# Kernel optimization log

Hardware: AMD Instinct MI355X
Metric: run time of the kernel (lower is better)

Reference implementation:

```python
import jax, jax.numpy as jnp
import numpy as np

B, S, V, I, H = 32, 512, 8000, 256, 512
LN_EPS = 1e-5


def setup_inputs() -> dict:
    key = jax.random.key(0)
    ks = jax.random.split(key, 8)
    norm = lambda k, shp, sc: jax.random.normal(k, shp, dtype=jnp.float32) * sc
    return {
        "x_idx": jax.random.randint(ks[0], (B, S), 0, V),
        "emb": norm(ks[1], (V, I), 1.0),                    # nn.Embedding weight
        "W_in": norm(ks[2], (H, I), 1.0 / np.sqrt(I)),       # input_proj
        "b_in": jnp.zeros((H,), jnp.float32),
        "W_rec": norm(ks[3], (H, H), 1.0 / np.sqrt(H)),      # recurrent_proj
        "b_rec": jnp.zeros((H,), jnp.float32),
        "W_tr": norm(ks[4], (H, H), 1.0 / np.sqrt(H)),       # trunk linear
        "b_tr": jnp.zeros((H,), jnp.float32),
        "gamma": jnp.ones((H,), jnp.float32),                # shared LayerNorm
        "beta": jnp.zeros((H,), jnp.float32),
        "W_out": norm(ks[5], (V, H), 1.0 / np.sqrt(H)),      # output_proj
        "b_out": jnp.zeros((V,), jnp.float32),
    }


def reference(x_idx, emb, W_in, b_in, W_rec, b_rec, W_tr, b_tr, gamma, beta, W_out, b_out):
    bsz = x_idx.shape[0]

    def layer_norm(x):
        m = jnp.mean(x, axis=-1, keepdims=True)
        v = jnp.mean((x - m) ** 2, axis=-1, keepdims=True)
        return (x - m) * jax.lax.rsqrt(v + LN_EPS) * gamma + beta

    xs = emb[x_idx]                     # [B,S,I] gather all embeddings up front
    xs_t = jnp.swapaxes(xs, 0, 1)       # [S,B,I] for scan over time

    def step(h, x_t):
        h_t = jnp.tanh(x_t @ W_in.T + b_in + h @ W_rec.T + b_rec)   # [B,H]
        h_new = layer_norm(jnp.tanh(h_t @ W_tr.T + b_tr))           # trunk (layer_count=1)
        return h_new, h_new

    h0 = jnp.zeros((bsz, W_in.shape[0]), xs.dtype)
    _, hs = jax.lax.scan(step, h0, xs_t)                            # hs: [S,B,H]

    # output projection is out of the recurrence -> batch it after the scan
    y_s = jnp.einsum('sbh,vh->bsv', hs, W_out) + b_out              # [B,S,V]
    return y_s
```

## Files before the change

kernel.cpp:

```cpp
#include <hip/hip_runtime.h>
#include <hip/hip_bf16.h>

#define B_ 32
#define S_ 512
#define V_ 8000
#define I_ 256
#define H_ 512
#define LN_EPS 1e-5f
#define NSL 16
#define NBP 8
#define NBLK 128
#define PHALF (NBLK * 2048)

#define OFF_WR   0
#define OFF_WT   16512
#define OFF_HB   33024
#define OFF_HTS  35088
#define OFF_RED  35220
#define OFF_RED2 37268
#define OFF_MISC 37284
#define LDSF     37288

typedef __attribute__((ext_vector_type(4))) float f32x4;
typedef __attribute__((ext_vector_type(8))) short short8;

static __device__ __forceinline__ unsigned short f2bf(float x) {
    __hip_bfloat16 h = __float2bfloat16(x);
    return *reinterpret_cast<unsigned short*>(&h);
}

__global__ void k_transpose(const float* __restrict__ in, float* __restrict__ out,
                            int R, int C) {
    __shared__ float tile[32][33];
    int c0 = blockIdx.x * 32, r0 = blockIdx.y * 32;
    int tx = threadIdx.x, ty = threadIdx.y;
#pragma unroll
    for (int i = 0; i < 32; i += 8)
        tile[ty + i][tx] = in[(size_t)(r0 + ty + i) * C + (c0 + tx)];
    __syncthreads();
#pragma unroll
    for (int i = 0; i < 32; i += 8)
        out[(size_t)(c0 + ty + i) * R + (r0 + tx)] = tile[tx][ty + i];
}

__global__ __launch_bounds__(256) void k_cvt_bf16(const float* __restrict__ in,
                                                  unsigned short* __restrict__ out, int n4) {
    for (int i = blockIdx.x * 256 + threadIdx.x; i < n4; i += gridDim.x * 256) {
        float4 v = ((const float4*)in)[i];
        ushort4 o;
        o.x = f2bf(v.x); o.y = f2bf(v.y); o.z = f2bf(v.z); o.w = f2bf(v.w);
        ((ushort4*)out)[i] = o;
    }
}

__global__ __launch_bounds__(512) void k_embed_proj(
        const int* __restrict__ x_idx, const float* __restrict__ emb,
        const float* __restrict__ WinT, const float* __restrict__ b_in,
        float* __restrict__ Xp) {
    __shared__ float e[8][I_];
    const int m0 = blockIdx.x * 8;
    const int t = threadIdx.x;
    {
        int r = t >> 6, i4 = (t & 63) * 4;
        int m = m0 + r;
        int s = m >> 5, b = m & 31;
        int idx = x_idx[b * S_ + s];
        *(float4*)&e[r][i4] = *(const float4*)&emb[(size_t)idx * I_ + i4];
    }
    __syncthreads();
    const int j = t;
    float acc[8];
    const float bj = b_in[j];
#pragma unroll
    for (int r = 0; r < 8; ++r) acc[r] = bj;
    for (int i = 0; i < I_; ++i) {
        float w = WinT[(size_t)i * H_ + j];
#pragma unroll
        for (int r = 0; r < 8; ++r) acc[r] += e[r][i] * w;
    }
#pragma unroll
    for (int r = 0; r < 8; ++r)
        Xp[(size_t)(m0 + r) * H_ + j] = acc[r];
}

__global__ __launch_bounds__(512, 2) void k_scan_xcd2(
        const float* __restrict__ Xp,
        const float* __restrict__ W_rec, const float* __restrict__ b_rec,
        const float* __restrict__ W_tr,  const float* __restrict__ b_tr,
        const float* __restrict__ gamma, const float* __restrict__ beta,
        float* __restrict__ pP, unsigned int* __restrict__ flags,
        unsigned int* __restrict__ xccs, unsigned short* __restrict__ hsB) {
    extern __shared__ float sm[];
    float*  WrS  = sm + OFF_WR;
    float*  WtS  = sm + OFF_WT;
    float*  hb   = sm + OFF_HB;
    float*  hts  = sm + OFF_HTS;
    float*  red  = sm + OFF_RED;
    float2* red2 = (float2*)(sm + OFF_RED2);

    const int bid = blockIdx.x;
    const int g = bid >> 3, bp = bid & 7;
    const int t = threadIdx.x;
    const int j = t & 31, kc = t >> 5;
    const int rB = t >> 7, jB = (t & 127) << 2;
    const int wid = t >> 6;

    for (int idx = t; idx < 32 * 512; idx += 512) {
        int jj = idx >> 9, k = idx & 511;
        WrS[jj * 516 + k] = W_rec[(size_t)(g * 32 + jj) * H_ + k];
    }
    for (int idx = t; idx < 512 * 32; idx += 512) {
        int jj = idx >> 5, kl = idx & 31;
        WtS[kl * 516 + jj] = W_tr[(size_t)jj * H_ + g * 32 + kl];
    }
    const float brj = b_rec[g * 32 + j];
    const float4 bt4 = *(const float4*)&b_tr[jB];
    const float4 gm4 = *(const float4*)&gamma[jB];
    const float4 be4 = *(const float4*)&beta[jB];

    unsigned xcc;
    asm volatile("s_getreg_b32 %0, hwreg(HW_REG_XCC_ID)" : "=s"(xcc));
    xcc &= 0xffu;
    if (t == 0)
        __hip_atomic_store(&xccs[bid], xcc, __ATOMIC_RELAXED, __HIP_MEMORY_SCOPE_AGENT);
    {
        int ok = 1;
        if (t < NSL) {
            unsigned v;
            do {
                v = __hip_atomic_load(&xccs[t * 8 + bp],
                                      __ATOMIC_RELAXED, __HIP_MEMORY_SCOPE_AGENT);
                if (v == 0xFFFFFFFFu) __builtin_amdgcn_s_sleep(1);
            } while (v == 0xFFFFFFFFu);
            ok = (v == xcc) ? 1 : 0;
        }
        unsigned long long bal = __ballot(ok);
        if (t == 0)
            ((int*)sm)[OFF_MISC] = (bal == ~0ull) ? 1 : 0;
    }
    __syncthreads();
    const bool fast = ((int*)sm)[OFF_MISC] != 0;

    for (int s = 0; s < S_; ++s) {
        float xv = 0.f;
        if (t < 128) xv = Xp[((size_t)s * B_ + bp * 4 + (t >> 5)) * H_ + g * 32 + (t & 31)];

        {
            float a0 = 0, a1 = 0, a2 = 0, a3 = 0;
            if (s > 0) {
                const int kbase = kc * 32;
#pragma unroll
                for (int i = 0; i < 8; ++i) {
                    const int k4 = kbase + i * 4;
                    const float4 w4 = *(const float4*)&WrS[j * 516 + k4];
                    const float4 h0 = *(const float4*)&hb[0 * 516 + k4];
                    const float4 h1 = *(const float4*)&hb[1 * 516 + k4];
                    const float4 h2 = *(const float4*)&hb[2 * 516 + k4];
                    const float4 h3 = *(const float4*)&hb[3 * 516 + k4];
                    a0 += h0.x * w4.x + h0.y * w4.y + h0.z * w4.z + h0.w * w4.w;
                    a1 += h1.x * w4.x + h1.y * w4.y + h1.z * w4.z + h1.w * w4.w;
                    a2 += h2.x * w4.x + h2.y * w4.y + h2.z * w4.z + h2.w * w4.w;
                    a3 += h3.x * w4.x + h3.y * w4.y + h3.z * w4.z + h3.w * w4.w;
                }
            }
            red[kc * 128 + 0 * 32 + j] = a0;
            red[kc * 128 + 1 * 32 + j] = a1;
            red[kc * 128 + 2 * 32 + j] = a2;
            red[kc * 128 + 3 * 32 + j] = a3;
        }
        __syncthreads();
        if (t < 128) {
            const int r2 = t >> 5, j2 = t & 31;
            float sum = 0.f;
#pragma unroll
            for (int c = 0; c < 16; ++c) sum += red[c * 128 + r2 * 32 + j2];
            hts[r2 * 33 + j2] = tanhf(sum + xv + brj);
        }
        __syncthreads();

        float4 pa = {0.f, 0.f, 0.f, 0.f};
        {
            const float* hrow = hts + rB * 33;
#pragma unroll 8
            for (int kl = 0; kl < 32; ++kl) {
                const float hv = hrow[kl];
                const float4 w4 = *(const float4*)&WtS[kl * 516 + jB];
                pa.x += hv * w4.x; pa.y += hv * w4.y;
                pa.z += hv * w4.z; pa.w += hv * w4.w;
            }
        }
        {
            float* pdst = pP + (size_t)(s & 1) * PHALF
                        + (size_t)bp * 32768 + g * 2048 + (rB * 512 + jB);
            if (fast) {
                f32x4 pv = {pa.x, pa.y, pa.z, pa.w};
                asm volatile("global_store_dwordx4 %0, %1, off sc0"
                             :: "v"(pdst), "v"(pv) : "memory");
            } else {
                union { float2 f; unsigned long long u; } q0, q1;
                q0.f = make_float2(pa.x, pa.y);
                q1.f = make_float2(pa.z, pa.w);
                __hip_atomic_store((unsigned long long*)pdst, q0.u,
                                   __ATOMIC_RELAXED, __HIP_MEMORY_SCOPE_AGENT);
                __hip_atomic_store((unsigned long long*)pdst + 1, q1.u,
                                   __ATOMIC_RELAXED, __HIP_MEMORY_SCOPE_AGENT);
            }
        }
        asm volatile("s_waitcnt vmcnt(0)" ::: "memory");
        __syncthreads();

        if (t == 0)
            __hip_atomic_store(&flags[(bp * 16 + g) * 16], (unsigned)(s + 1),
                               __ATOMIC_RELEASE, __HIP_MEMORY_SCOPE_AGENT);
        if (t < NSL)
            while (__hip_atomic_load(&flags[(bp * 16 + t) * 16],
                       __ATOMIC_RELAXED, __HIP_MEMORY_SCOPE_AGENT) < (unsigned)(s + 1))
                __builtin_amdgcn_s_sleep(1);
        __syncthreads();
        __builtin_amdgcn_sched_barrier(0);

        f32x4 vv[16];
        {
            const float* gbase = pP + (size_t)(s & 1) * PHALF
                               + (size_t)bp * 32768 + (rB * 512 + jB);
            if (fast) {
#pragma unroll
                for (int gg = 0; gg < 16; ++gg)
                    asm volatile("global_load_dwordx4 %0, %1, off sc0"
                                 : "=v"(vv[gg]) : "v"(gbase + gg * 2048) : "memory");
                asm volatile("s_waitcnt vmcnt(0)" ::: "memory");
                __builtin_amdgcn_sched_barrier(0);
            } else {
#pragma unroll
                for (int gg = 0; gg < 16; ++gg) {
                    const unsigned long long* bp64 =
                        (const unsigned long long*)(gbase + gg * 2048);
                    unsigned long long v0 = __hip_atomic_load(bp64,
                        __ATOMIC_RELAXED, __HIP_MEMORY_SCOPE_AGENT);
                    unsigned long long v1 = __hip_atomic_load(bp64 + 1,
                        __ATOMIC_RELAXED, __HIP_MEMORY_SCOPE_AGENT);
                    union { unsigned long long u; float2 f; } w0, w1;
                    w0.u = v0; w1.u = v1;
                    vv[gg] = (f32x4){w0.f.x, w0.f.y, w1.f.x, w1.f.y};
                }
            }
        }
        float u0, u1, u2, u3;
        {
            float a0 = 0, a1 = 0, a2 = 0, a3 = 0;
#pragma unroll
            for (int gg = 0; gg < 16; ++gg) {
                a0 += vv[gg].x; a1 += vv[gg].y; a2 += vv[gg].z; a3 += vv[gg].w;
            }
            u0 = tanhf(a0 + bt4.x); u1 = tanhf(a1 + bt4.y);
            u2 = tanhf(a2 + bt4.z); u3 = tanhf(a3 + bt4.w);
            float s1 = (u0 + u1) + (u2 + u3);
            float s2 = (u0 * u0 + u1 * u1) + (u2 * u2 + u3 * u3);
#pragma unroll
            for (int o = 1; o < 64; o <<= 1) {
                s1 += __shfl_xor(s1, o);
                s2 += __shfl_xor(s2, o);
            }
            if ((t & 63) == 0) red2[wid] = make_float2(s1, s2);
        }
        __syncthreads();

        {
            const float2 A = red2[rB * 2], Bv = red2[rB * 2 + 1];
            const float mean = (A.x + Bv.x) * (1.0f / H_);
            const float var  = (A.y + Bv.y) * (1.0f / H_) - mean * mean;
            const float rs = rsqrtf(var + LN_EPS);
            float4 hn;
            hn.x = (u0 - mean) * rs * gm4.x + be4.x;
            hn.y = (u1 - mean) * rs * gm4.y + be4.y;
            hn.z = (u2 - mean) * rs * gm4.z + be4.z;
            hn.w = (u3 - mean) * rs * gm4.w + be4.w;
            *(float4*)&hb[rB * 516 + jB] = hn;
            if ((jB >> 5) == g) {
                ushort4 o;
                o.x = f2bf(hn.x); o.y = f2bf(hn.y);
                o.z = f2bf(hn.z); o.w = f2bf(hn.w);
                *(ushort4*)&hsB[((size_t)s * B_ + bp * 4 + rB) * H_ + jB] = o;
            }
        }
        __syncthreads();
    }
}

__global__ __launch_bounds__(256) void k_out_mfma(
        const unsigned short* __restrict__ hsB, const unsigned short* __restrict__ WoB,
        const float* __restrict__ b_out, float* __restrict__ y) {
    __shared__ unsigned short As[128 * 40];
    __shared__ unsigned short Bs[128 * 40];

    const int v0 = blockIdx.x * 128;
    const int m0 = blockIdx.y * 128;
    const int t = threadIdx.x;
    const int l = t & 63, wv = t >> 6;
    const int wm = wv >> 1, wn = wv & 1;

    f32x4 acc[4][4];
#pragma unroll
    for (int i = 0; i < 4; ++i)
#pragma unroll
        for (int jq = 0; jq < 4; ++jq)
            acc[i][jq] = (f32x4){0.f, 0.f, 0.f, 0.f};

    float bias[4];
#pragma unroll
    for (int ni = 0; ni < 4; ++ni) {
        int v = v0 + wn * 64 + ni * 16 + (l & 15);
        bias[ni] = (v < V_) ? b_out[v] : 0.f;
    }

    for (int k0 = 0; k0 < H_; k0 += 32) {
        __syncthreads();
        for (int c = t; c < 512; c += 256) {
            int row = c >> 2, seg = c & 3;
            *(uint4*)&As[row * 40 + seg * 8] =
                *(const uint4*)&hsB[(size_t)(m0 + row) * H_ + k0 + seg * 8];
            int vr = v0 + row; if (vr > V_ - 1) vr = V_ - 1;
            *(uint4*)&Bs[row * 40 + seg * 8] =
                *(const uint4*)&WoB[(size_t)vr * H_ + k0 + seg * 8];
        }
        __syncthreads();

        short8 af[4], bf[4];
#pragma unroll
        for (int i = 0; i < 4; ++i) {
            af[i] = *(short8*)&As[(wm * 64 + i * 16 + (l & 15)) * 40 + (l >> 4) * 8];
            bf[i] = *(short8*)&Bs[(wn * 64 + i * 16 + (l & 15)) * 40 + (l >> 4) * 8];
        }
#pragma unroll
        for (int mi = 0; mi < 4; ++mi)
#pragma unroll
            for (int ni = 0; ni < 4; ++ni)
                acc[mi][ni] = __builtin_amdgcn_mfma_f32_16x16x32_bf16(
                    af[mi], bf[ni], acc[mi][ni], 0, 0, 0);
    }

#pragma unroll
    for (int mi = 0; mi < 4; ++mi) {
#pragma unroll
        for (int ni = 0; ni < 4; ++ni) {
            int vcol = v0 + wn * 64 + ni * 16 + (l & 15);
            if (vcol < V_) {
#pragma unroll
                for (int p = 0; p < 4; ++p) {
                    int m = m0 + wm * 64 + mi * 16 + (l >> 4) * 4 + p;
                    int s = m >> 5, b = m & 31;
                    y[((size_t)b * S_ + s) * V_ + vcol] = acc[mi][ni][p] + bias[ni];
                }
            }
        }
    }
}

extern "C" void kernel_launch(void* const* d_in, const int* in_sizes, int n_in,
                              void* d_out, int out_size, void* d_ws, size_t ws_size,
                              hipStream_t stream) {
    const int*   x_idx = (const int*)d_in[0];
    const float* emb   = (const float*)d_in[1];
    const float* W_in  = (const float*)d_in[2];
    const float* b_in  = (const float*)d_in[3];
    const float* W_rec = (const float*)d_in[4];
    const float* b_rec = (const float*)d_in[5];
    const float* W_tr  = (const float*)d_in[6];
    const float* b_tr  = (const float*)d_in[7];
    const float* gamma = (const float*)d_in[8];
    const float* beta  = (const float*)d_in[9];
    const float* W_out = (const float*)d_in[10];
    const float* b_out = (const float*)d_in[11];
    float* y  = (float*)d_out;
    float* ws = (float*)d_ws;

    float* WinT = ws;
    float* Xp   = ws + 131072;
    unsigned short* hsB = (unsigned short*)(ws + 8519680);
    unsigned short* WoB = (unsigned short*)(ws + 12713984);
    float* pP   = ws + 14761984;
    unsigned int* flags = (unsigned int*)(ws + 15286272);
    unsigned int* xccs  = (unsigned int*)(ws + 15288320);

    (void)hipFuncSetAttribute((const void*)k_scan_xcd2,
                              hipFuncAttributeMaxDynamicSharedMemorySize,
                              LDSF * 4);

    dim3 tb(32, 8);
    k_transpose<<<dim3(I_ / 32, H_ / 32), tb, 0, stream>>>(W_in, WinT, H_, I_);

    k_cvt_bf16<<<1024, 256, 0, stream>>>(W_out, WoB, V_ * H_ / 4);

    k_embed_proj<<<(B_ * S_) / 8, 512, 0, stream>>>(x_idx, emb, WinT, b_in, Xp);

    hipMemsetAsync(flags, 0, 2048 * sizeof(unsigned int), stream);
    hipMemsetAsync(xccs, 0xFF, 128 * sizeof(unsigned int), stream);

    k_scan_xcd2<<<NBLK, 512, LDSF * 4, stream>>>(Xp, W_rec, b_rec, W_tr, b_tr,
                                                 gamma, beta, pP, flags, xccs, hsB);

    k_out_mfma<<<dim3((V_ + 127) / 128, (B_ * S_) / 128), 256, 0, stream>>>(
        hsB, WoB, b_out, y);
}
```

Measured before the change: 3.828 ms.

## Split scan across 256 blocks with two batch rows per block group

The recurrent scan kernel now runs on 256 blocks instead of 128. Each group of 16 column-slice blocks handles 2 batch rows instead of 4, so per-block work per timestep halves: the recurrent dot products, the trunk partials, the partial exchange through global memory and the LayerNorm all shrink. The aim is to shorten the serial per-step latency by using more CUs. In exchange the kernel needs more co-resident blocks, each loads its own full copy of the weight slices, and there are more flag and partial-buffer locations to synchronise on.

```diff
diff --git a/kernel.cpp b/kernel.cpp
--- a/kernel.cpp
+++ b/kernel.cpp
@@ -8,20 +8,21 @@
 #define H_ 512
 #define LN_EPS 1e-5f
 #define NSL 16
-#define NBP 8
-#define NBLK 128
-#define PHALF (NBLK * 2048)
+#define NBP 16
+#define NBLK 256
+#define PHALF 262144
 
 #define OFF_WR   0
 #define OFF_WT   16512
 #define OFF_HB   33024
-#define OFF_HTS  35088
-#define OFF_RED  35220
-#define OFF_RED2 37268
-#define OFF_MISC 37284
-#define LDSF     37288
+#define OFF_HTS  34056
+#define OFF_RED  34124
+#define OFF_RED2 35148
+#define OFF_MISC 35164
+#define LDSF     35168
 
 typedef __attribute__((ext_vector_type(4))) float f32x4;
+typedef __attribute__((ext_vector_type(2))) float f32x2;
 typedef __attribute__((ext_vector_type(8))) short short8;
 
 static __device__ __forceinline__ unsigned short f2bf(float x) {
@@ -83,7 +84,7 @@
         Xp[(size_t)(m0 + r) * H_ + j] = acc[r];
 }
 
-__global__ __launch_bounds__(512, 2) void k_scan_xcd2(
+__global__ __launch_bounds__(512, 2) void k_scan_v4(
         const float* __restrict__ Xp,
         const float* __restrict__ W_rec, const float* __restrict__ b_rec,
         const float* __restrict__ W_tr,  const float* __restrict__ b_tr,
@@ -99,10 +100,10 @@
     float2* red2 = (float2*)(sm + OFF_RED2);
 
     const int bid = blockIdx.x;
-    const int g = bid >> 3, bp = bid & 7;
+    const int g = bid >> 4, rp = bid & 15;
     const int t = threadIdx.x;
     const int j = t & 31, kc = t >> 5;
-    const int rB = t >> 7, jB = (t & 127) << 2;
+    const int rB = t >> 8, jB = (t & 255) << 1;
     const int wid = t >> 6;
 
     for (int idx = t; idx < 32 * 512; idx += 512) {
@@ -114,9 +115,9 @@
         WtS[kl * 516 + jj] = W_tr[(size_t)jj * H_ + g * 32 + kl];
     }
     const float brj = b_rec[g * 32 + j];
-    const float4 bt4 = *(const float4*)&b_tr[jB];
-    const float4 gm4 = *(const float4*)&gamma[jB];
-    const float4 be4 = *(const float4*)&beta[jB];
+    const float2 bt2 = *(const float2*)&b_tr[jB];
+    const float2 gm2 = *(const float2*)&gamma[jB];
+    const float2 be2 = *(const float2*)&beta[jB];
 
     unsigned xcc;
     asm volatile("s_getreg_b32 %0, hwreg(HW_REG_XCC_ID)" : "=s"(xcc));
@@ -128,7 +129,7 @@
         if (t < NSL) {
             unsigned v;
             do {
-                v = __hip_atomic_load(&xccs[t * 8 + bp],
+                v = __hip_atomic_load(&xccs[t * 16 + rp],
                                       __ATOMIC_RELAXED, __HIP_MEMORY_SCOPE_AGENT);
                 if (v == 0xFFFFFFFFu) __builtin_amdgcn_s_sleep(1);
             } while (v == 0xFFFFFFFFu);
@@ -143,10 +144,10 @@
 
     for (int s = 0; s < S_; ++s) {
         float xv = 0.f;
-        if (t < 128) xv = Xp[((size_t)s * B_ + bp * 4 + (t >> 5)) * H_ + g * 32 + (t & 31)];
-
-        {
-            float a0 = 0, a1 = 0, a2 = 0, a3 = 0;
+        if (t < 64) xv = Xp[((size_t)s * B_ + rp * 2 + (t >> 5)) * H_ + g * 32 + (t & 31)];
+
+        {
+            float a0 = 0, a1 = 0;
             if (s > 0) {
                 const int kbase = kc * 32;
 #pragma unroll
@@ -155,107 +156,91 @@
                     const float4 w4 = *(const float4*)&WrS[j * 516 + k4];
                     const float4 h0 = *(const float4*)&hb[0 * 516 + k4];
                     const float4 h1 = *(const float4*)&hb[1 * 516 + k4];
-                    const float4 h2 = *(const float4*)&hb[2 * 516 + k4];
-                    const float4 h3 = *(const float4*)&hb[3 * 516 + k4];
                     a0 += h0.x * w4.x + h0.y * w4.y + h0.z * w4.z + h0.w * w4.w;
                     a1 += h1.x * w4.x + h1.y * w4.y + h1.z * w4.z + h1.w * w4.w;
-                    a2 += h2.x * w4.x + h2.y * w4.y + h2.z * w4.z + h2.w * w4.w;
-                    a3 += h3.x * w4.x + h3.y * w4.y + h3.z * w4.z + h3.w * w4.w;
                 }
             }
-            red[kc * 128 + 0 * 32 + j] = a0;
-            red[kc * 128 + 1 * 32 + j] = a1;
-            red[kc * 128 + 2 * 32 + j] = a2;
-            red[kc * 128 + 3 * 32 + j] = a3;
-        }
-        __syncthreads();
-        if (t < 128) {
+            red[kc * 64 + 0 * 32 + j] = a0;
+            red[kc * 64 + 1 * 32 + j] = a1;
+        }
+        __syncthreads();
+        if (t < 64) {
             const int r2 = t >> 5, j2 = t & 31;
             float sum = 0.f;
 #pragma unroll
-            for (int c = 0; c < 16; ++c) sum += red[c * 128 + r2 * 32 + j2];
+            for (int c = 0; c < 16; ++c) sum += red[c * 64 + r2 * 32 + j2];
             hts[r2 * 33 + j2] = tanhf(sum + xv + brj);
         }
         __syncthreads();
 
-        float4 pa = {0.f, 0.f, 0.f, 0.f};
+        float pa0 = 0.f, pa1 = 0.f;
         {
             const float* hrow = hts + rB * 33;
 #pragma unroll 8
             for (int kl = 0; kl < 32; ++kl) {
                 const float hv = hrow[kl];
-                const float4 w4 = *(const float4*)&WtS[kl * 516 + jB];
-                pa.x += hv * w4.x; pa.y += hv * w4.y;
-                pa.z += hv * w4.z; pa.w += hv * w4.w;
+                const float2 w2 = *(const float2*)&WtS[kl * 516 + jB];
+                pa0 += hv * w2.x; pa1 += hv * w2.y;
             }
         }
         {
             float* pdst = pP + (size_t)(s & 1) * PHALF
-                        + (size_t)bp * 32768 + g * 2048 + (rB * 512 + jB);
+                        + (size_t)rp * 16384 + g * 1024 + (rB * 512 + jB);
             if (fast) {
-                f32x4 pv = {pa.x, pa.y, pa.z, pa.w};
-                asm volatile("global_store_dwordx4 %0, %1, off sc0"
+                f32x2 pv = {pa0, pa1};
+                asm volatile("global_store_dwordx2 %0, %1, off sc0"
                              :: "v"(pdst), "v"(pv) : "memory");
             } else {
-                union { float2 f; unsigned long long u; } q0, q1;
-                q0.f = make_float2(pa.x, pa.y);
-                q1.f = make_float2(pa.z, pa.w);
+                union { float2 f; unsigned long long u; } q0;
+                q0.f = make_float2(pa0, pa1);
                 __hip_atomic_store((unsigned long long*)pdst, q0.u,
                                    __ATOMIC_RELAXED, __HIP_MEMORY_SCOPE_AGENT);
-                __hip_atomic_store((unsigned long long*)pdst + 1, q1.u,
-                                   __ATOMIC_RELAXED, __HIP_MEMORY_SCOPE_AGENT);
             }
         }
         asm volatile("s_waitcnt vmcnt(0)" ::: "memory");
         __syncthreads();
 
         if (t == 0)
-            __hip_atomic_store(&flags[(bp * 16 + g) * 16], (unsigned)(s + 1),
+            __hip_atomic_store(&flags[(rp * 16 + g) * 16], (unsigned)(s + 1),
                                __ATOMIC_RELEASE, __HIP_MEMORY_SCOPE_AGENT);
         if (t < NSL)
-            while (__hip_atomic_load(&flags[(bp * 16 + t) * 16],
+            while (__hip_atomic_load(&flags[(rp * 16 + t) * 16],
                        __ATOMIC_RELAXED, __HIP_MEMORY_SCOPE_AGENT) < (unsigned)(s + 1))
                 __builtin_amdgcn_s_sleep(1);
         __syncthreads();
         __builtin_amdgcn_sched_barrier(0);
 
-        f32x4 vv[16];
+        f32x2 vv[16];
         {
             const float* gbase = pP + (size_t)(s & 1) * PHALF
-                               + (size_t)bp * 32768 + (rB * 512 + jB);
+                               + (size_t)rp * 16384 + (rB * 512 + jB);
             if (fast) {
 #pragma unroll
                 for (int gg = 0; gg < 16; ++gg)
-                    asm volatile("global_load_dwordx4 %0, %1, off sc0"
-                                 : "=v"(vv[gg]) : "v"(gbase + gg * 2048) : "memory");
+                    asm volatile("global_load_dwordx2 %0, %1, off sc0"
+                                 : "=v"(vv[gg]) : "v"(gbase + gg * 1024) : "memory");
                 asm volatile("s_waitcnt vmcnt(0)" ::: "memory");
                 __builtin_amdgcn_sched_barrier(0);
             } else {
 #pragma unroll
                 for (int gg = 0; gg < 16; ++gg) {
-                    const unsigned long long* bp64 =
-                        (const unsigned long long*)(gbase + gg * 2048);
-                    unsigned long long v0 = __hip_atomic_load(bp64,
+                    unsigned long long v0 = __hip_atomic_load(
+                        (const unsigned long long*)(gbase + gg * 1024),
                         __ATOMIC_RELAXED, __HIP_MEMORY_SCOPE_AGENT);
-                    unsigned long long v1 = __hip_atomic_load(bp64 + 1,
-                        __ATOMIC_RELAXED, __HIP_MEMORY_SCOPE_AGENT);
-                    union { unsigned long long u; float2 f; } w0, w1;
-                    w0.u = v0; w1.u = v1;
-                    vv[gg] = (f32x4){w0.f.x, w0.f.y, w1.f.x, w1.f.y};
+                    union { unsigned long long u; float2 f; } w0;
+                    w0.u = v0;
+                    vv[gg] = (f32x2){w0.f.x, w0.f.y};
                 }
             }
         }
-        float u0, u1, u2, u3;
-        {
-            float a0 = 0, a1 = 0, a2 = 0, a3 = 0;
-#pragma unroll
-            for (int gg = 0; gg < 16; ++gg) {
-                a0 += vv[gg].x; a1 += vv[gg].y; a2 += vv[gg].z; a3 += vv[gg].w;
-            }
-            u0 = tanhf(a0 + bt4.x); u1 = tanhf(a1 + bt4.y);
-            u2 = tanhf(a2 + bt4.z); u3 = tanhf(a3 + bt4.w);
-            float s1 = (u0 + u1) + (u2 + u3);
-            float s2 = (u0 * u0 + u1 * u1) + (u2 * u2 + u3 * u3);
+        float u0, u1;
+        {
+            float a0 = 0, a1 = 0;
+#pragma unroll
+            for (int gg = 0; gg < 16; ++gg) { a0 += vv[gg].x; a1 += vv[gg].y; }
+            u0 = tanhf(a0 + bt2.x); u1 = tanhf(a1 + bt2.y);
+            float s1 = u0 + u1;
+            float s2 = u0 * u0 + u1 * u1;
 #pragma unroll
             for (int o = 1; o < 64; o <<= 1) {
                 s1 += __shfl_xor(s1, o);
@@ -266,21 +251,18 @@
         __syncthreads();
 
         {
-            const float2 A = red2[rB * 2], Bv = red2[rB * 2 + 1];
-            const float mean = (A.x + Bv.x) * (1.0f / H_);
-            const float var  = (A.y + Bv.y) * (1.0f / H_) - mean * mean;
+            const float2 A0 = red2[rB * 4 + 0], A1 = red2[rB * 4 + 1];
+            const float2 A2 = red2[rB * 4 + 2], A3 = red2[rB * 4 + 3];
+            const float mean = ((A0.x + A1.x) + (A2.x + A3.x)) * (1.0f / H_);
+            const float var  = ((A0.y + A1.y) + (A2.y + A3.y)) * (1.0f / H_) - mean * mean;
             const float rs = rsqrtf(var + LN_EPS);
-            float4 hn;
-            hn.x = (u0 - mean) * rs * gm4.x + be4.x;
-            hn.y = (u1 - mean) * rs * gm4.y + be4.y;
-            hn.z = (u2 - mean) * rs * gm4.z + be4.z;
-            hn.w = (u3 - mean) * rs * gm4.w + be4.w;
-            *(float4*)&hb[rB * 516 + jB] = hn;
+            float hn0 = (u0 - mean) * rs * gm2.x + be2.x;
+            float hn1 = (u1 - mean) * rs * gm2.y + be2.y;
+            *(float2*)&hb[rB * 516 + jB] = make_float2(hn0, hn1);
             if ((jB >> 5) == g) {
-                ushort4 o;
-                o.x = f2bf(hn.x); o.y = f2bf(hn.y);
-                o.z = f2bf(hn.z); o.w = f2bf(hn.w);
-                *(ushort4*)&hsB[((size_t)s * B_ + bp * 4 + rB) * H_ + jB] = o;
+                ushort2 o;
+                o.x = f2bf(hn0); o.y = f2bf(hn1);
+                *(ushort2*)&hsB[((size_t)s * B_ + rp * 2 + rB) * H_ + jB] = o;
             }
         }
         __syncthreads();
@@ -380,9 +362,9 @@
     unsigned short* WoB = (unsigned short*)(ws + 12713984);
     float* pP   = ws + 14761984;
     unsigned int* flags = (unsigned int*)(ws + 15286272);
-    unsigned int* xccs  = (unsigned int*)(ws + 15288320);
-
-    (void)hipFuncSetAttribute((const void*)k_scan_xcd2,
+    unsigned int* xccs  = (unsigned int*)(ws + 15290368);
+
+    (void)hipFuncSetAttribute((const void*)k_scan_v4,
                               hipFuncAttributeMaxDynamicSharedMemorySize,
                               LDSF * 4);
 
@@ -393,11 +375,11 @@
 
     k_embed_proj<<<(B_ * S_) / 8, 512, 0, stream>>>(x_idx, emb, WinT, b_in, Xp);
 
-    hipMemsetAsync(flags, 0, 2048 * sizeof(unsigned int), stream);
-    hipMemsetAsync(xccs, 0xFF, 128 * sizeof(unsigned int), stream);
-
-    k_scan_xcd2<<<NBLK, 512, LDSF * 4, stream>>>(Xp, W_rec, b_rec, W_tr, b_tr,
-                                                 gamma, beta, pP, flags, xccs, hsB);
+    hipMemsetAsync(flags, 0, 4096 * sizeof(unsigned int), stream);
+    hipMemsetAsync(xccs, 0xFF, 256 * sizeof(unsigned int), stream);
+
+    k_scan_v4<<<NBLK, 512, LDSF * 4, stream>>>(Xp, W_rec, b_rec, W_tr, b_tr,
+                                               gamma, beta, pP, flags, xccs, hsB);
 
     k_out_mfma<<<dim3((V_ + 127) / 128, (B_ * S_) / 128), 256, 0, stream>>>(
         hsB, WoB, b_out, y);
```

After: 4.049 ms. 1.06x slower.
